# Optimization experiments

Measured on AMD Instinct MI355X. Metric: run time of the kernel, lower is better.

## Reference

```python
import jax, jax.numpy as jnp
import numpy as np

N = 50000
E = 800000
IN = 256
HEADS = 8
C = 32  # out_size // heads
OUT = HEADS * C
NEG_SLOPE = 0.2
LN_EPS = 1e-5


def setup_inputs() -> dict:
    key = jax.random.key(0)
    ks = jax.random.split(key, 6)
    x = jax.random.normal(ks[0], (N, IN), dtype=jnp.float32)
    edge_index = jax.random.randint(ks[1], (2, E), 0, N, dtype=jnp.int64)
    W = jax.random.normal(ks[2], (IN, OUT), dtype=jnp.float32) / np.sqrt(IN)
    att_src = jax.random.normal(ks[3], (HEADS, C), dtype=jnp.float32) / np.sqrt(C)
    att_dst = jax.random.normal(ks[4], (HEADS, C), dtype=jnp.float32) / np.sqrt(C)
    bias = jnp.zeros((OUT,), dtype=jnp.float32)
    ln_gamma = jnp.ones((OUT,), dtype=jnp.float32)
    ln_beta = jnp.zeros((OUT,), dtype=jnp.float32)
    return {"x": x, "edge_index": edge_index, "W": W, "att_src": att_src,
            "att_dst": att_dst, "bias": bias, "ln_gamma": ln_gamma, "ln_beta": ln_beta}


def _gat_layer(x, src, dst, W, att_src, att_dst, bias, ln_gamma, ln_beta):
    n = x.shape[0]
    h = (x @ W).reshape(n, HEADS, C)                      # [N,H,C]
    a_src = jnp.sum(h * att_src[None], axis=-1)           # [N,H]
    a_dst = jnp.sum(h * att_dst[None], axis=-1)           # [N,H]
    e = a_src[src] + a_dst[dst]                           # [Etot,H]
    e = jnp.where(e > 0, e, NEG_SLOPE * e)                # LeakyReLU(0.2)
    # segment softmax over incoming edges of each dst node
    emax = jax.lax.stop_gradient(jax.ops.segment_max(e, dst, num_segments=n))
    ex = jnp.exp(e - emax[dst])
    denom = jax.ops.segment_sum(ex, dst, num_segments=n)
    alpha = ex / denom[dst]                               # [Etot,H]
    msg = h[src] * alpha[:, :, None]                      # [Etot,H,C]
    out = jax.ops.segment_sum(msg, dst, num_segments=n).reshape(n, OUT) + bias
    # LayerNorm
    mu = jnp.mean(out, axis=-1, keepdims=True)
    var = jnp.var(out, axis=-1, keepdims=True)
    out = (out - mu) * jax.lax.rsqrt(var + LN_EPS) * ln_gamma + ln_beta
    return jax.nn.relu(out)


def reference(x, edge_index, W, att_src, att_dst, bias, ln_gamma, ln_beta):
    n = x.shape[0]
    loops = jnp.arange(n, dtype=edge_index.dtype)
    src = jnp.concatenate([edge_index[0], loops])  # PyG GATConv adds self-loops
    dst = jnp.concatenate([edge_index[1], loops])
    return _gat_layer(x, src, dst, W, att_src, att_dst, bias, ln_gamma, ln_beta)
```

## Files before the change

kernel.cpp:

```cpp
#include <hip/hip_runtime.h>

#define NEG 0.2f
#define ELLW 64

typedef __attribute__((ext_vector_type(8))) __bf16 bf16x8;
typedef __attribute__((ext_vector_type(4))) float f32x4;

__device__ __forceinline__ unsigned short f2bf(float f) {
    unsigned int u = __float_as_uint(f);
    u += 0x7FFFu + ((u >> 16) & 1u);
    return (unsigned short)(u >> 16);
}

__global__ __launch_bounds__(256) void prep_kernel(const float* __restrict__ W,
                                                   unsigned short* __restrict__ Wt,
                                                   const float* __restrict__ x,
                                                   unsigned short* __restrict__ xb,
                                                   int* __restrict__ len, int N) {
    int b = blockIdx.x, t = threadIdx.x;
    if (b < 256) {
        Wt[b * 256 + t] = f2bf(W[t * 256 + b]);
        int idx = b * 256 + t;
        if (idx < N) len[idx] = 0;
        return;
    }
    size_t base = (size_t)(b - 256) * 2048 + (size_t)t * 8;
    size_t total = (size_t)N * 256;
    if (base < total) {
        float4 v0 = *(const float4*)(x + base);
        float4 v1 = *(const float4*)(x + base + 4);
        uint4 p;
        p.x = (unsigned int)f2bf(v0.x) | ((unsigned int)f2bf(v0.y) << 16);
        p.y = (unsigned int)f2bf(v0.z) | ((unsigned int)f2bf(v0.w) << 16);
        p.z = (unsigned int)f2bf(v1.x) | ((unsigned int)f2bf(v1.y) << 16);
        p.w = (unsigned int)f2bf(v1.z) | ((unsigned int)f2bf(v1.w) << 16);
        *(uint4*)(xb + base) = p;
    }
}

struct SmemGemm { unsigned short A[64][40]; unsigned short B[256][40]; };
struct SmemEpi  { float asrc[64][9]; float adst[64][9]; };
union SmemU { SmemGemm g; SmemEpi e; };

__global__ __launch_bounds__(256) void gemm_ell(const unsigned short* __restrict__ xb,
                                                const unsigned short* __restrict__ Wt,
                                                unsigned short* __restrict__ h,
                                                const float* __restrict__ att_src,
                                                const float* __restrict__ att_dst,
                                                float* __restrict__ a_src,
                                                float* __restrict__ a_dst, int nrows, int G,
                                                const int* __restrict__ ei,
                                                int* __restrict__ len,
                                                int* __restrict__ ell, int E) {
    __shared__ SmemU sm;

    if (blockIdx.x >= G) {
        int base = (blockIdx.x - G) * 2048 + threadIdx.x;
        int s0 = -1, s1 = -1, s2 = -1, s3 = -1, s4 = -1, s5 = -1, s6 = -1, s7 = -1;
        int d0 = 0, d1 = 0, d2 = 0, d3 = 0, d4 = 0, d5 = 0, d6 = 0, d7 = 0;
#define ELOAD(K, SK, DK) { int e_ = base + (K) * 256; \
        if (e_ < E) { SK = ei[e_]; DK = ei[E + e_]; } }
        ELOAD(0, s0, d0) ELOAD(1, s1, d1) ELOAD(2, s2, d2) ELOAD(3, s3, d3)
        ELOAD(4, s4, d4) ELOAD(5, s5, d5) ELOAD(6, s6, d6) ELOAD(7, s7, d7)
#undef ELOAD
        int t0 = 0, t1 = 0, t2 = 0, t3 = 0, t4 = 0, t5 = 0, t6 = 0, t7 = 0;
        if (s0 >= 0) t0 = atomicAdd(&len[d0], 1);
        if (s1 >= 0) t1 = atomicAdd(&len[d1], 1);
        if (s2 >= 0) t2 = atomicAdd(&len[d2], 1);
        if (s3 >= 0) t3 = atomicAdd(&len[d3], 1);
        if (s4 >= 0) t4 = atomicAdd(&len[d4], 1);
        if (s5 >= 0) t5 = atomicAdd(&len[d5], 1);
        if (s6 >= 0) t6 = atomicAdd(&len[d6], 1);
        if (s7 >= 0) t7 = atomicAdd(&len[d7], 1);
        if (s0 >= 0 && t0 < ELLW) ell[d0 * ELLW + t0] = s0;
        if (s1 >= 0 && t1 < ELLW) ell[d1 * ELLW + t1] = s1;
        if (s2 >= 0 && t2 < ELLW) ell[d2 * ELLW + t2] = s2;
        if (s3 >= 0 && t3 < ELLW) ell[d3 * ELLW + t3] = s3;
        if (s4 >= 0 && t4 < ELLW) ell[d4 * ELLW + t4] = s4;
        if (s5 >= 0 && t5 < ELLW) ell[d5 * ELLW + t5] = s5;
        if (s6 >= 0 && t6 < ELLW) ell[d6 * ELLW + t6] = s6;
        if (s7 >= 0 && t7 < ELLW) ell[d7 * ELLW + t7] = s7;
        return;
    }

    int t = threadIdx.x;
    int lane = t & 63, wave = t >> 6;
    int row0 = blockIdx.x * 64;

    f32x4 acc[4][4] = {};

    for (int kk = 0; kk < 8; ++kk) {
        int k0 = kk * 32;
        {
            int r = t >> 2, cg = (t & 3) * 8;
            int gr = row0 + r;
            uint4 av = make_uint4(0u, 0u, 0u, 0u);
            if (gr < nrows) av = *(const uint4*)(xb + (size_t)gr * 256 + k0 + cg);
            *(uint4*)&sm.g.A[r][cg] = av;
        }
        {
            const uint4* src = (const uint4*)(Wt + (size_t)t * 256 + k0);
            uint4 b0 = src[0], b1 = src[1], b2 = src[2], b3 = src[3];
            *(uint4*)&sm.g.B[t][0]  = b0;
            *(uint4*)&sm.g.B[t][8]  = b1;
            *(uint4*)&sm.g.B[t][16] = b2;
            *(uint4*)&sm.g.B[t][24] = b3;
        }
        __syncthreads();

        int fr = lane & 15, fk = (lane >> 4) * 8;
        bf16x8 a[4];
#pragma unroll
        for (int mi = 0; mi < 4; ++mi) a[mi] = *(const bf16x8*)&sm.g.A[mi * 16 + fr][fk];
#pragma unroll
        for (int ni = 0; ni < 4; ++ni) {
            bf16x8 b = *(const bf16x8*)&sm.g.B[wave * 64 + ni * 16 + fr][fk];
#pragma unroll
            for (int mi = 0; mi < 4; ++mi)
                acc[mi][ni] = __builtin_amdgcn_mfma_f32_16x16x32_bf16(a[mi], b, acc[mi][ni], 0, 0, 0);
        }
        __syncthreads();
    }

    int cr = (lane >> 4) * 4;
    int cc = lane & 15;
#pragma unroll
    for (int mi = 0; mi < 4; ++mi)
#pragma unroll
        for (int ni = 0; ni < 4; ++ni)
#pragma unroll
            for (int r = 0; r < 4; ++r) {
                int row = row0 + mi * 16 + cr + r;
                int col = wave * 64 + ni * 16 + cc;
                if (row < nrows) h[(size_t)row * 256 + col] = f2bf(acc[mi][ni][r]);
            }

    float avs[4], avd[4];
#pragma unroll
    for (int ni = 0; ni < 4; ++ni) {
        int col = wave * 64 + ni * 16 + cc;
        avs[ni] = att_src[col];
        avd[ni] = att_dst[col];
    }
#pragma unroll
    for (int mi = 0; mi < 4; ++mi)
#pragma unroll
        for (int r = 0; r < 4; ++r) {
            float s0 = acc[mi][0][r] * avs[0] + acc[mi][1][r] * avs[1];
            float s1 = acc[mi][2][r] * avs[2] + acc[mi][3][r] * avs[3];
            float d0 = acc[mi][0][r] * avd[0] + acc[mi][1][r] * avd[1];
            float d1 = acc[mi][2][r] * avd[2] + acc[mi][3][r] * avd[3];
#pragma unroll
            for (int o = 1; o < 16; o <<= 1) {
                s0 += __shfl_xor(s0, o, 64);
                s1 += __shfl_xor(s1, o, 64);
                d0 += __shfl_xor(d0, o, 64);
                d1 += __shfl_xor(d1, o, 64);
            }
            if (cc == 0) {
                int row = mi * 16 + cr + r;
                sm.e.asrc[row][wave * 2 + 0] = s0;
                sm.e.asrc[row][wave * 2 + 1] = s1;
                sm.e.adst[row][wave * 2 + 0] = d0;
                sm.e.adst[row][wave * 2 + 1] = d1;
            }
        }
    __syncthreads();
    for (int idx = t; idx < 512; idx += 256) {
        int row = idx >> 3, hd = idx & 7;
        if (row0 + row < nrows) {
            a_src[(size_t)(row0 + row) * 8 + hd] = sm.e.asrc[row][hd];
            a_dst[(size_t)(row0 + row) * 8 + hd] = sm.e.adst[row][hd];
        }
    }
}

__device__ __forceinline__ void fma8(f32x4& a0, f32x4& a1, float al, uint4 u) {
    a0[0] = fmaf(al, __uint_as_float(u.x << 16),         a0[0]);
    a0[1] = fmaf(al, __uint_as_float(u.x & 0xffff0000u), a0[1]);
    a0[2] = fmaf(al, __uint_as_float(u.y << 16),         a0[2]);
    a0[3] = fmaf(al, __uint_as_float(u.y & 0xffff0000u), a0[3]);
    a1[0] = fmaf(al, __uint_as_float(u.z << 16),         a1[0]);
    a1[1] = fmaf(al, __uint_as_float(u.z & 0xffff0000u), a1[1]);
    a1[2] = fmaf(al, __uint_as_float(u.w << 16),         a1[2]);
    a1[3] = fmaf(al, __uint_as_float(u.w & 0xffff0000u), a1[3]);
}

__global__ __launch_bounds__(256, 6) void agg_kernel(const unsigned short* __restrict__ h,
                                                     const float* __restrict__ a_src,
                                                     const float* __restrict__ a_dst,
                                                     const int* __restrict__ len,
                                                     const int* __restrict__ ell,
                                                     const float* __restrict__ bias,
                                                     const float* __restrict__ gamma,
                                                     const float* __restrict__ beta,
                                                     float* __restrict__ out, int N) {
    __shared__ float alL[4][ELLW][8];

    int lane = threadIdx.x & 63, wave = threadIdx.x >> 6;
    int i = blockIdx.x * 4 + wave;
    if (i >= N) return;

    volatile float (*al)[8] = alL[wave];

    int deg = len[i];
    deg = deg < ELLW ? deg : ELLW;
    int dm1 = deg - 1;

    int sreg = (lane < deg) ? ell[i * ELLW + lane] : 0;

    int hh = lane & 7, jj = lane >> 3;
    float adh = a_dst[i * 8 + hh];
    float es = a_src[i * 8 + hh] + adh;
    es = es > 0.f ? es : NEG * es;
    float selfexp = __expf(es);

    float sum = (jj == 0) ? selfexp : 0.f;
    for (int jb = 0; jb < deg; jb += 8) {
        int j = jb + jj;
        int jc = j < deg ? j : dm1;
        int s = __shfl(sreg, jc, 64);
        float e = a_src[s * 8 + hh] + adh;
        e = e > 0.f ? e : NEG * e;
        float v = __expf(e);
        if (j < deg) {
            al[j][hh] = v;
            sum += v;
        }
    }
    sum += __shfl_xor(sum, 8, 64);
    sum += __shfl_xor(sum, 16, 64);
    sum += __shfl_xor(sum, 32, 64);
    float ginv = 1.0f / sum;

    __builtin_amdgcn_wave_barrier();

    int sub = lane >> 5, l5 = lane & 31;
    int c0 = l5 * 8;
    int hl = l5 >> 2;
    float gv = __shfl(ginv, hl, 64);
    float sv = __shfl(selfexp, hl, 64);

    f32x4 a0 = {0.f, 0.f, 0.f, 0.f}, a1 = {0.f, 0.f, 0.f, 0.f};
    if (deg > 0) {
#define P2LOAD(jb, AL, U) { \
        int j_ = (jb) + sub; \
        int jc_ = j_ < deg ? j_ : dm1; \
        int s_ = __shfl(sreg, jc_, 64); \
        AL = (j_ < deg ? al[jc_][hl] : 0.f) * gv; \
        U = *(const uint4*)(h + (size_t)s_ * 256 + c0); }

        float alA, alB;
        uint4 uA, uB;
        P2LOAD(0, alA, uA)
        P2LOAD(2, alB, uB)
        int jb = 0;
        for (; jb + 4 < deg; jb += 4) {
            fma8(a0, a1, alA, uA); P2LOAD(jb + 4, alA, uA)
            fma8(a0, a1, alB, uB); P2LOAD(jb + 6, alB, uB)
        }
        fma8(a0, a1, alA, uA);
        fma8(a0, a1, alB, uB);
#undef P2LOAD
    }
    {
        float alphaS = (sub == 1) ? sv * gv : 0.f;
        uint4 us = *(const uint4*)(h + (size_t)i * 256 + c0);
        fma8(a0, a1, alphaS, us);
    }
#pragma unroll
    for (int k = 0; k < 4; ++k) {
        a0[k] += __shfl_xor(a0[k], 32, 64);
        a1[k] += __shfl_xor(a1[k], 32, 64);
    }

    float4 b0 = *(const float4*)(bias + c0);
    float4 b1 = *(const float4*)(bias + c0 + 4);
    float o0 = a0[0] + b0.x, o1 = a0[1] + b0.y, o2 = a0[2] + b0.z, o3 = a0[3] + b0.w;
    float o4 = a1[0] + b1.x, o5 = a1[1] + b1.y, o6 = a1[2] + b1.z, o7 = a1[3] + b1.w;

    float s1 = o0 + o1 + o2 + o3 + o4 + o5 + o6 + o7;
    float s2 = o0 * o0 + o1 * o1 + o2 * o2 + o3 * o3
             + o4 * o4 + o5 * o5 + o6 * o6 + o7 * o7;
#pragma unroll
    for (int off = 16; off >= 1; off >>= 1) {
        s1 += __shfl_xor(s1, off, 64);
        s2 += __shfl_xor(s2, off, 64);
    }
    float mean = s1 * (1.f / 256.f);
    float var = s2 * (1.f / 256.f) - mean * mean;
    float rstd = rsqrtf(var + 1e-5f);

    float4 g0 = *(const float4*)(gamma + c0);
    float4 g1 = *(const float4*)(gamma + c0 + 4);
    float4 t0 = *(const float4*)(beta + c0);
    float4 t1 = *(const float4*)(beta + c0 + 4);

    f32x4 w0, w1;
    w0[0] = fmaxf((o0 - mean) * rstd * g0.x + t0.x, 0.f);
    w0[1] = fmaxf((o1 - mean) * rstd * g0.y + t0.y, 0.f);
    w0[2] = fmaxf((o2 - mean) * rstd * g0.z + t0.z, 0.f);
    w0[3] = fmaxf((o3 - mean) * rstd * g0.w + t0.w, 0.f);
    w1[0] = fmaxf((o4 - mean) * rstd * g1.x + t1.x, 0.f);
    w1[1] = fmaxf((o5 - mean) * rstd * g1.y + t1.y, 0.f);
    w1[2] = fmaxf((o6 - mean) * rstd * g1.z + t1.z, 0.f);
    w1[3] = fmaxf((o7 - mean) * rstd * g1.w + t1.w, 0.f);

    float* op = out + (size_t)i * 256 + c0;
    if (sub == 0) *(f32x4*)op       = w0;
    else          *(f32x4*)(op + 4) = w1;
}

extern "C" void kernel_launch(void* const* d_in, const int* in_sizes, int n_in,
                              void* d_out, int out_size, void* d_ws, size_t ws_size,
                              hipStream_t stream) {
    const float* x       = (const float*)d_in[0];
    const int*   ei      = (const int*)d_in[1];
    const float* W       = (const float*)d_in[2];
    const float* att_src = (const float*)d_in[3];
    const float* att_dst = (const float*)d_in[4];
    const float* bias    = (const float*)d_in[5];
    const float* gamma   = (const float*)d_in[6];
    const float* beta    = (const float*)d_in[7];

    int N = in_sizes[0] / 256;
    int E = in_sizes[1] / 2;
    int G = (N + 63) / 64;
    int EB = (E + 2047) / 2048;
    int XB = ((N * 256 + 2047) / 2048);

    char* ws = (char*)d_ws;
    size_t off = 0;
    auto alloc = [&](size_t bytes) -> void* {
        void* p = ws + off;
        off += (bytes + 255) & ~(size_t)255;
        return p;
    };
    unsigned short* Wt     = (unsigned short*)alloc((size_t)256 * 256 * 2);
    unsigned short* xb     = (unsigned short*)alloc((size_t)N * 256 * 2);
    unsigned short* h      = (unsigned short*)alloc((size_t)N * 256 * 2);
    float*          a_src_ = (float*)alloc((size_t)N * 8 * 4);
    float*          a_dst_ = (float*)alloc((size_t)N * 8 * 4);
    int*            len    = (int*)alloc((size_t)N * 4);
    int*            ell    = (int*)alloc((size_t)N * ELLW * 4);

    prep_kernel<<<256 + XB, 256, 0, stream>>>(W, Wt, x, xb, len, N);
    gemm_ell<<<G + EB, 256, 0, stream>>>(xb, Wt, h, att_src, att_dst, a_src_, a_dst_, N, G,
                                         ei, len, ell, E);
    agg_kernel<<<(N + 3) / 4, 256, 0, stream>>>(h, a_src_, a_dst_, len, ell, bias, gamma, beta,
                                                (float*)d_out, N);
}
```

Before: 249.6 us.

## Split GEMM output columns across two blocks and prefetch next K tile into registers

Each GEMM block now computes a 64x128 output tile instead of 64x256, so twice as many blocks run, and the LDS tile for W shrinks by half. Global loads for the next K slice go into registers before the MFMA work of the current slice, overlapping memory latency with compute. The cost is that each x row tile is loaded twice, once per column half, and there is an extra barrier per iteration. The attention-score epilogue is reworked so each block writes the four heads it owns.

```diff
diff --git a/kernel.cpp b/kernel.cpp
--- a/kernel.cpp
+++ b/kernel.cpp
@@ -38,8 +38,8 @@
     }
 }
 
-struct SmemGemm { unsigned short A[64][40]; unsigned short B[256][40]; };
-struct SmemEpi  { float asrc[64][9]; float adst[64][9]; };
+struct SmemGemm { unsigned short A[64][40]; unsigned short B[128][40]; };
+struct SmemEpi  { float asrc[64][5]; float adst[64][5]; };
 union SmemU { SmemGemm g; SmemEpi e; };
 
 __global__ __launch_bounds__(256) void gemm_ell(const unsigned short* __restrict__ xb,
@@ -85,60 +85,67 @@
 
     int t = threadIdx.x;
     int lane = t & 63, wave = t >> 6;
-    int row0 = blockIdx.x * 64;
-
-    f32x4 acc[4][4] = {};
+    int rowtile = blockIdx.x >> 1, ch = blockIdx.x & 1;
+    int row0 = rowtile * 64;
+    int colbase = ch * 128;
+
+    f32x4 acc[4][2] = {};
+
+    int ar = t >> 2, acg = (t & 3) * 8;
+    int agr = row0 + ar;
+    const unsigned short* arow = xb + (size_t)agr * 256 + acg;
+    int br = t >> 1, bk = (t & 1) * 16;
+    const unsigned short* wrow = Wt + (size_t)(colbase + br) * 256 + bk;
+
+    uint4 aR = make_uint4(0u, 0u, 0u, 0u), b0R, b1R;
+    if (agr < nrows) aR = *(const uint4*)(arow);
+    b0R = *(const uint4*)(wrow);
+    b1R = *(const uint4*)(wrow + 8);
 
     for (int kk = 0; kk < 8; ++kk) {
-        int k0 = kk * 32;
-        {
-            int r = t >> 2, cg = (t & 3) * 8;
-            int gr = row0 + r;
-            uint4 av = make_uint4(0u, 0u, 0u, 0u);
-            if (gr < nrows) av = *(const uint4*)(xb + (size_t)gr * 256 + k0 + cg);
-            *(uint4*)&sm.g.A[r][cg] = av;
-        }
-        {
-            const uint4* src = (const uint4*)(Wt + (size_t)t * 256 + k0);
-            uint4 b0 = src[0], b1 = src[1], b2 = src[2], b3 = src[3];
-            *(uint4*)&sm.g.B[t][0]  = b0;
-            *(uint4*)&sm.g.B[t][8]  = b1;
-            *(uint4*)&sm.g.B[t][16] = b2;
-            *(uint4*)&sm.g.B[t][24] = b3;
-        }
         __syncthreads();
-
+        *(uint4*)&sm.g.A[ar][acg]    = aR;
+        *(uint4*)&sm.g.B[br][bk]     = b0R;
+        *(uint4*)&sm.g.B[br][bk + 8] = b1R;
+        __syncthreads();
+        if (kk < 7) {
+            int k0 = (kk + 1) * 32;
+            aR = make_uint4(0u, 0u, 0u, 0u);
+            if (agr < nrows) aR = *(const uint4*)(arow + k0);
+            b0R = *(const uint4*)(wrow + k0);
+            b1R = *(const uint4*)(wrow + k0 + 8);
+        }
         int fr = lane & 15, fk = (lane >> 4) * 8;
         bf16x8 a[4];
 #pragma unroll
         for (int mi = 0; mi < 4; ++mi) a[mi] = *(const bf16x8*)&sm.g.A[mi * 16 + fr][fk];
 #pragma unroll
-        for (int ni = 0; ni < 4; ++ni) {
-            bf16x8 b = *(const bf16x8*)&sm.g.B[wave * 64 + ni * 16 + fr][fk];
+        for (int ni = 0; ni < 2; ++ni) {
+            bf16x8 b = *(const bf16x8*)&sm.g.B[wave * 32 + ni * 16 + fr][fk];
 #pragma unroll
             for (int mi = 0; mi < 4; ++mi)
                 acc[mi][ni] = __builtin_amdgcn_mfma_f32_16x16x32_bf16(a[mi], b, acc[mi][ni], 0, 0, 0);
         }
-        __syncthreads();
-    }
+    }
+    __syncthreads();
 
     int cr = (lane >> 4) * 4;
     int cc = lane & 15;
 #pragma unroll
     for (int mi = 0; mi < 4; ++mi)
 #pragma unroll
-        for (int ni = 0; ni < 4; ++ni)
+        for (int ni = 0; ni < 2; ++ni)
 #pragma unroll
             for (int r = 0; r < 4; ++r) {
                 int row = row0 + mi * 16 + cr + r;
-                int col = wave * 64 + ni * 16 + cc;
+                int col = colbase + wave * 32 + ni * 16 + cc;
                 if (row < nrows) h[(size_t)row * 256 + col] = f2bf(acc[mi][ni][r]);
             }
 
-    float avs[4], avd[4];
-#pragma unroll
-    for (int ni = 0; ni < 4; ++ni) {
-        int col = wave * 64 + ni * 16 + cc;
+    float avs[2], avd[2];
+#pragma unroll
+    for (int ni = 0; ni < 2; ++ni) {
+        int col = colbase + wave * 32 + ni * 16 + cc;
         avs[ni] = att_src[col];
         avd[ni] = att_dst[col];
     }
@@ -146,31 +153,25 @@
     for (int mi = 0; mi < 4; ++mi)
 #pragma unroll
         for (int r = 0; r < 4; ++r) {
-            float s0 = acc[mi][0][r] * avs[0] + acc[mi][1][r] * avs[1];
-            float s1 = acc[mi][2][r] * avs[2] + acc[mi][3][r] * avs[3];
-            float d0 = acc[mi][0][r] * avd[0] + acc[mi][1][r] * avd[1];
-            float d1 = acc[mi][2][r] * avd[2] + acc[mi][3][r] * avd[3];
+            float s = acc[mi][0][r] * avs[0] + acc[mi][1][r] * avs[1];
+            float d = acc[mi][0][r] * avd[0] + acc[mi][1][r] * avd[1];
 #pragma unroll
             for (int o = 1; o < 16; o <<= 1) {
-                s0 += __shfl_xor(s0, o, 64);
-                s1 += __shfl_xor(s1, o, 64);
-                d0 += __shfl_xor(d0, o, 64);
-                d1 += __shfl_xor(d1, o, 64);
+                s += __shfl_xor(s, o, 64);
+                d += __shfl_xor(d, o, 64);
             }
             if (cc == 0) {
                 int row = mi * 16 + cr + r;
-                sm.e.asrc[row][wave * 2 + 0] = s0;
-                sm.e.asrc[row][wave * 2 + 1] = s1;
-                sm.e.adst[row][wave * 2 + 0] = d0;
-                sm.e.adst[row][wave * 2 + 1] = d1;
+                sm.e.asrc[row][wave] = s;
+                sm.e.adst[row][wave] = d;
             }
         }
     __syncthreads();
-    for (int idx = t; idx < 512; idx += 256) {
-        int row = idx >> 3, hd = idx & 7;
+    {
+        int row = t >> 2, w = t & 3;
         if (row0 + row < nrows) {
-            a_src[(size_t)(row0 + row) * 8 + hd] = sm.e.asrc[row][hd];
-            a_dst[(size_t)(row0 + row) * 8 + hd] = sm.e.adst[row][hd];
+            a_src[(size_t)(row0 + row) * 8 + ch * 4 + w] = sm.e.asrc[row][w];
+            a_dst[(size_t)(row0 + row) * 8 + ch * 4 + w] = sm.e.adst[row][w];
         }
     }
 }
@@ -325,7 +326,7 @@
 
     int N = in_sizes[0] / 256;
     int E = in_sizes[1] / 2;
-    int G = (N + 63) / 64;
+    int G = 2 * ((N + 63) / 64);
     int EB = (E + 2047) / 2048;
     int XB = ((N * 256 + 2047) / 2048);
 
```

New measurement: 252.2 us. No clear change (+1.0%).
